# Kernel optimization log

Hardware: AMD Instinct MI355X
Metric: run time of the kernel (lower is better)

The kernel has to match this reference:

```python
import jax, jax.numpy as jnp
import numpy as np

N, B, D = 2048, 4, 512
H, DH = 8, 64
INNER = H * DH
EPS = 1e-5


def _layernorm(x, g, b):
    mu = jnp.mean(x, axis=-1, keepdims=True)
    var = jnp.var(x, axis=-1, keepdims=True)
    return (x - mu) * jax.lax.rsqrt(var + EPS) * g + b


def setup_inputs() -> dict:
    key = jax.random.key(0)
    ks = jax.random.split(key, 5)
    inp = {
        "x": jax.random.normal(ks[0], (N, B, D), jnp.float32),
        "kv": jax.random.normal(ks[1], (N, B, D), jnp.float32),
        # weights stored as [in, out] (jax convention; transpose of torch Linear.weight)
        "Wq": jax.random.normal(ks[2], (D, INNER), jnp.float32) * (D ** -0.5),
        "Wkv": jax.random.normal(ks[3], (D, INNER), jnp.float32) * (D ** -0.5),
        "ln_q_g": jnp.ones((DH,), jnp.float32),
        "ln_q_b": jnp.zeros((DH,), jnp.float32),
        "Wo": jax.random.normal(ks[4], (INNER, D), jnp.float32) * (INNER ** -0.5),
        "bo": jnp.zeros((D,), jnp.float32),
        "ln_o_g": jnp.ones((D,), jnp.float32),
        "ln_o_b": jnp.zeros((D,), jnp.float32),
        "ls_scale": jnp.full((1, 1, D), EPS, jnp.float32),  # LayerScale init eps=1e-5
    }
    return inp


def reference(x, kv, Wq, Wkv, ln_q_g, ln_q_b, Wo, bo, ln_o_g, ln_o_b, ls_scale):
    n = x.shape[0]
    xb = jnp.transpose(x, (1, 0, 2))    # (b, n, d)
    kvb = jnp.transpose(kv, (1, 0, 2))  # (b, m, d)
    b = xb.shape[0]
    q = xb @ Wq                          # (b, n, inner)
    kvp = kvb @ Wkv                      # (b, m, inner)
    q = q.reshape(b, n, H, DH).transpose(0, 2, 1, 3)         # (b, h, n, dh)
    kvp = kvp.reshape(b, -1, H, DH).transpose(0, 2, 1, 3)    # (b, h, m, dh)
    q = _layernorm(q, ln_q_g, ln_q_b)
    sim = jnp.einsum('bhnd,bhmd->bhnm', q, kvp) * (DH ** -0.5)
    attn = jax.nn.softmax(sim, axis=-1)
    out = jnp.einsum('bhnm,bhmd->bhnd', attn, kvp)           # KV shared as value
    out = out.transpose(0, 2, 1, 3).reshape(b, n, INNER)
    out = _layernorm(out @ Wo + bo, ln_o_g, ln_o_b)          # to_out: Linear + LN
    out = jnp.transpose(out, (1, 0, 2))                       # (n, b, d)
    return ls_scale * out
```

## Files before the change

kernel.cpp:

```cpp
#include <hip/hip_runtime.h>

#define NN 2048
#define BB 4
#define DD 512
#define HH 8
#define DHH 64
#define RR 8192

#define SCALE_L2E (0.125f * 1.44269504088896340736f)

typedef __attribute__((ext_vector_type(8))) __bf16 bf16x8;
typedef __attribute__((ext_vector_type(2))) float f32x2;
typedef __attribute__((ext_vector_type(4))) float f32x4;
typedef __attribute__((ext_vector_type(16))) float f32x16;
typedef __attribute__((ext_vector_type(2))) unsigned int u32x2;
typedef __attribute__((ext_vector_type(4))) unsigned int u32x4;

static __device__ __forceinline__ unsigned short f2bf(float f) {
  unsigned u = __builtin_bit_cast(unsigned, f);
  u += 0x7fffu + ((u >> 16) & 1u);
  return (unsigned short)(u >> 16);
}

static __device__ __forceinline__ unsigned cvtpk(float lo, float hi) {
  unsigned r;
  asm("v_cvt_pk_bf16_f32 %0, %1, %2" : "=v"(r) : "v"(lo), "v"(hi));
  return r;
}

#define PAIR(v, i) __builtin_shufflevector(v, v, 2 * (i), 2 * (i) + 1)

static __device__ __forceinline__ void g2l16(const void* g, void* l) {
  __builtin_amdgcn_global_load_lds((const __attribute__((address_space(1))) unsigned int*)g,
                                   (__attribute__((address_space(3))) unsigned int*)l, 16, 0, 0);
}

static __device__ __forceinline__ int swz(int row, int col) {
  return (row * 32 + col) ^ (((row >> 1) & 3) << 3);
}

__global__ __launch_bounds__(256) void cast_all_kernel(
    const float* __restrict__ x, const float* __restrict__ kv,
    const float* __restrict__ Wq, const float* __restrict__ Wkv, const float* __restrict__ Wo,
    unsigned short* __restrict__ xb, unsigned short* __restrict__ kvb,
    unsigned short* __restrict__ WqT, unsigned short* __restrict__ WkvT,
    unsigned short* __restrict__ WoT) {
  int bid = blockIdx.x;
  if (bid < 4096) {
    const float* src = (bid >= 2048) ? kv : x;
    unsigned short* dst = (bid >= 2048) ? kvb : xb;
    int t = (bid & 2047) * 256 + threadIdx.x;
    int o0 = t * 8;
    int d = o0 & 511;
    int n = (o0 >> 9) & 2047;
    int b = o0 >> 20;
    const float* s = src + ((size_t)(n * BB + b) << 9) + d;
    f32x4 v0 = *(const f32x4*)s;
    f32x4 v1 = *(const f32x4*)(s + 4);
    union { unsigned short us[8]; u32x4 v; } o;
#pragma unroll
    for (int i = 0; i < 4; ++i) { o.us[i] = f2bf(v0[i]); o.us[4 + i] = f2bf(v1[i]); }
    *(u32x4*)(dst + o0) = o.v;
  } else {
    int wi = bid - 4096;
    int which = wi >> 10;
    const float* W = (which == 0) ? Wq : (which == 1) ? Wkv : Wo;
    unsigned short* WT = (which == 0) ? WqT : (which == 1) ? WkvT : WoT;
    int idx = (wi & 1023) * 256 + threadIdx.x;
    int o = idx & 511;
    int k = idx >> 9;
    WT[(size_t)o * 512 + k] = f2bf(W[(size_t)k * 512 + o]);
  }
}

#define GEMM_CORE(Aptr, WTptr)                                                        \
  __shared__ unsigned short At[2][128 * 32];                                          \
  __shared__ unsigned short Bt[2][128 * 32];                                          \
  int tid = threadIdx.x;                                                              \
  int w = tid >> 6, l = tid & 63, lr = l & 15, lh = l >> 4;                           \
  int wr = w >> 1, wc = w & 1;                                                        \
  int r0 = blockIdx.x * 128, c0 = blockIdx.y * 128;                                   \
  int chA = w * 2, chB = w * 2 + 1;                                                   \
  int rowA = chA * 16 + (l >> 2), rowB = chB * 16 + (l >> 2);                         \
  int cbA = ((l & 3) * 16) ^ (((rowA >> 1) & 3) << 4);                                \
  int cbB = ((l & 3) * 16) ^ (((rowB >> 1) & 3) << 4);                                \
  const char* sA0 = (const char*)(Aptr) + (size_t)(r0 + rowA) * 1024 + cbA;           \
  const char* sA1 = (const char*)(Aptr) + (size_t)(r0 + rowB) * 1024 + cbB;           \
  const char* sB0 = (const char*)(WTptr) + (size_t)(c0 + rowA) * 1024 + cbA;          \
  const char* sB1 = (const char*)(WTptr) + (size_t)(c0 + rowB) * 1024 + cbB;          \
  auto stageg = [&](int buf, int k0) {                                                \
    char* la = (char*)&At[buf][0] + chA * 1024;                                       \
    char* lb2 = (char*)&Bt[buf][0] + chA * 1024;                                      \
    g2l16(sA0 + k0 * 2, la);                                                          \
    g2l16(sA1 + k0 * 2, la + 1024);                                                   \
    g2l16(sB0 + k0 * 2, lb2);                                                         \
    g2l16(sB1 + k0 * 2, lb2 + 1024);                                                  \
  };                                                                                  \
  f32x4 acc[4][4] = {};                                                               \
  stageg(0, 0);                                                                       \
  __syncthreads();                                                                    \
  _Pragma("unroll")                                                                   \
  for (int i = 0; i < 16; ++i) {                                                      \
    int buf = i & 1;                                                                  \
    if (i < 15) stageg(buf ^ 1, i * 32 + 32);                                         \
    bf16x8 a[4], b[4];                                                                \
    _Pragma("unroll")                                                                 \
    for (int m = 0; m < 4; ++m)                                                       \
      a[m] = *(const bf16x8*)&At[buf][swz(wr * 64 + m * 16 + lr, lh * 8)];            \
    _Pragma("unroll")                                                                 \
    for (int n = 0; n < 4; ++n)                                                       \
      b[n] = *(const bf16x8*)&Bt[buf][swz(wc * 64 + n * 16 + lr, lh * 8)];            \
    _Pragma("unroll")                                                                 \
    for (int m = 0; m < 4; ++m)                                                       \
      _Pragma("unroll")                                                               \
      for (int n = 0; n < 4; ++n)                                                     \
        acc[m][n] = __builtin_amdgcn_mfma_f32_16x16x32_bf16(a[m], b[n], acc[m][n], 0, 0, 0); \
    __syncthreads();                                                                  \
  }

__global__ __launch_bounds__(256) void gemm01_kernel(
    const unsigned short* __restrict__ xb, const unsigned short* __restrict__ kvb,
    const unsigned short* __restrict__ WqT, const unsigned short* __restrict__ WkvT,
    const float* __restrict__ lnqg, const float* __restrict__ lnqb,
    unsigned short* __restrict__ qln, unsigned short* __restrict__ kvp,
    unsigned short* __restrict__ kvpT) {
  int z = blockIdx.z;
  const unsigned short* A = z ? kvb : xb;
  const unsigned short* WT = z ? WkvT : WqT;
  GEMM_CORE(A, WT)
  int row_base = r0 + wr * 64;
  int h = (c0 + wc * 64) >> 6;
  if (z == 0) {
    float gq[4], bq[4];
#pragma unroll
    for (int n = 0; n < 4; ++n) { gq[n] = lnqg[n * 16 + lr]; bq[n] = lnqb[n * 16 + lr]; }
#pragma unroll
    for (int m = 0; m < 4; ++m)
#pragma unroll
      for (int i = 0; i < 4; ++i) {
        float s1 = 0.f, s2 = 0.f;
#pragma unroll
        for (int n = 0; n < 4; ++n) { float v = acc[m][n][i]; s1 += v; s2 += v * v; }
#pragma unroll
        for (int off = 1; off < 16; off <<= 1) { s1 += __shfl_xor(s1, off); s2 += __shfl_xor(s2, off); }
        float mean = s1 * (1.f / 64.f);
        float var = s2 * (1.f / 64.f) - mean * mean;
        float rstd = rsqrtf(var + 1e-5f);
        int row = row_base + m * 16 + lh * 4 + i;
        int b = row >> 11, nidx = row & 2047;
        size_t obase = ((size_t)(b * HH + h) * NN + nidx) * DHH;
#pragma unroll
        for (int n = 0; n < 4; ++n) {
          float v = ((acc[m][n][i] - mean) * rstd * gq[n] + bq[n]) * SCALE_L2E;
          qln[obase + n * 16 + lr] = f2bf(v);
        }
      }
  } else {
#pragma unroll
    for (int m = 0; m < 4; ++m)
#pragma unroll
      for (int i = 0; i < 4; ++i) {
        int row = row_base + m * 16 + lh * 4 + i;
        int b = row >> 11, nidx = row & 2047;
        size_t obase = ((size_t)(b * HH + h) * NN + nidx) * DHH;
        size_t tbase = ((size_t)(b * HH + h) * DHH) * NN + nidx;
#pragma unroll
        for (int n = 0; n < 4; ++n) {
          unsigned short v = f2bf(acc[m][n][i]);
          int dh = n * 16 + lr;
          kvp[obase + dh] = v;
          kvpT[tbase + (size_t)dh * NN] = v;
        }
      }
  }
}

__global__ __launch_bounds__(256) void gemm2_kernel(
    const unsigned short* __restrict__ Ain,
    const unsigned short* __restrict__ WTin,
    const float* __restrict__ g,
    float* __restrict__ out_f32) {
  GEMM_CORE(Ain, WTin)
  int row_base = r0 + wr * 64;
#pragma unroll
  for (int m = 0; m < 4; ++m)
#pragma unroll
    for (int i = 0; i < 4; ++i) {
      int row = row_base + m * 16 + lh * 4 + i;
#pragma unroll
      for (int n = 0; n < 4; ++n) {
        int col = c0 + wc * 64 + n * 16 + lr;
        out_f32[(size_t)row * 512 + col] = acc[m][n][i] + g[col];
      }
    }
}

__global__ __launch_bounds__(128) void attn_kernel(
    const unsigned short* __restrict__ qb, const unsigned short* __restrict__ kb,
    const unsigned short* __restrict__ vtb, unsigned short* __restrict__ attn_out) {
  int bid = blockIdx.x;
  int xcd = bid & 7, idx = bid >> 3;
  int bh = xcd * 4 + (idx >> 5);
  int qt = idx & 31;
  int tid = threadIdx.x, w = tid >> 6, l = tid & 63;
  int q = l & 31, hi = l >> 5;
  const unsigned short* Q = qb + (size_t)bh * NN * DHH;
  const unsigned short* Kp = kb + (size_t)bh * NN * DHH;
  const unsigned short* VT = vtb + (size_t)bh * DHH * NN;
  int qr0 = qt * 64 + w * 32;

  __shared__ unsigned short kt_lds[2][64 * 64];
  __shared__ unsigned short vt_lds[2][64 * 64];

  int qswz = (q & 7) << 4;

  bf16x8 bq[4];
#pragma unroll
  for (int st = 0; st < 4; ++st)
    bq[st] = *(const bf16x8*)&Q[(size_t)(qr0 + q) * DHH + st * 16 + hi * 8];

  float lsum = 0.f;
  f32x16 o0 = {}, o1 = {};

  int rl = l >> 3;
  int scol = ((l & 7) << 4) ^ (rl << 4);
  auto stage = [&](int buf, int kt2) {
    int kr0 = kt2 * 64;
    if (w == 0) {
      char* lb = (char*)&kt_lds[buf][0];
      const char* gb = (const char*)(Kp + (size_t)kr0 * DHH);
#pragma unroll
      for (int p = 0; p < 8; ++p)
        g2l16(gb + (p * 8 + rl) * 128 + scol, lb + p * 1024);
    } else {
      char* lb = (char*)&vt_lds[buf][0];
      const char* gb = (const char*)VT + (size_t)kr0 * 2;
#pragma unroll
      for (int p = 0; p < 8; ++p)
        g2l16(gb + (size_t)(p * 8 + rl) * (NN * 2) + scol, lb + p * 1024);
    }
  };

  stage(0, 0);
  __syncthreads();

#pragma unroll 2
  for (int kt = 0; kt < 32; ++kt) {
    int cur = kt & 1;
    if (kt < 31) stage(cur ^ 1, kt + 1);
    const char* kbuf = (const char*)&kt_lds[cur][0];
    const char* vbuf = (const char*)&vt_lds[cur][0];

    f32x16 s0 = {}, s1 = {};
#pragma unroll
    for (int st = 0; st < 4; ++st) {
      int cb = (st * 32 + hi * 16) ^ qswz;
      bf16x8 a0 = *(const bf16x8*)(kbuf + q * 128 + cb);
      bf16x8 a1 = *(const bf16x8*)(kbuf + (q + 32) * 128 + cb);
      s0 = __builtin_amdgcn_mfma_f32_32x32x16_bf16(a0, bq[st], s0, 0, 0, 0);
      s1 = __builtin_amdgcn_mfma_f32_32x32x16_bf16(a1, bq[st], s1, 0, 0, 0);
    }

#pragma unroll
    for (int i = 0; i < 16; ++i) {
      s0[i] = exp2f(s0[i]);
      s1[i] = exp2f(s1[i]);
    }
    f32x2 t0 = PAIR(s0, 0) + PAIR(s0, 1), t1 = PAIR(s0, 2) + PAIR(s0, 3);
    f32x2 t2 = PAIR(s0, 4) + PAIR(s0, 5), t3 = PAIR(s0, 6) + PAIR(s0, 7);
    f32x2 u0 = PAIR(s1, 0) + PAIR(s1, 1), u1 = PAIR(s1, 2) + PAIR(s1, 3);
    f32x2 u2 = PAIR(s1, 4) + PAIR(s1, 5), u3 = PAIR(s1, 6) + PAIR(s1, 7);
    f32x2 vv = ((t0 + t1) + (t2 + t3)) + ((u0 + u1) + (u2 + u3));
    lsum += vv[0] + vv[1];

#pragma unroll
    for (int st = 0; st < 4; ++st) {
      const f32x16& sv = (st < 2) ? s0 : s1;
      int b0 = (st & 1) * 8;
      unsigned X0 = cvtpk(sv[b0 + 0], sv[b0 + 1]);
      unsigned X1 = cvtpk(sv[b0 + 2], sv[b0 + 3]);
      unsigned Y0 = cvtpk(sv[b0 + 4], sv[b0 + 5]);
      unsigned Y1 = cvtpk(sv[b0 + 6], sv[b0 + 7]);
      auto r0 = __builtin_amdgcn_permlane32_swap(X0, Y0, false, false);
      auto r1 = __builtin_amdgcn_permlane32_swap(X1, Y1, false, false);
      u32x4 pw;
      pw[0] = r0[0];
      pw[1] = r1[0];
      pw[2] = r0[1];
      pw[3] = r1[1];
      bf16x8 bp = __builtin_bit_cast(bf16x8, pw);
      int cb = (st * 32 + hi * 16) ^ qswz;
      bf16x8 va0 = *(const bf16x8*)(vbuf + q * 128 + cb);
      bf16x8 va1 = *(const bf16x8*)(vbuf + (q + 32) * 128 + cb);
      o0 = __builtin_amdgcn_mfma_f32_32x32x16_bf16(va0, bp, o0, 0, 0, 0);
      o1 = __builtin_amdgcn_mfma_f32_32x32x16_bf16(va1, bp, o1, 0, 0, 0);
    }
    __syncthreads();
  }

  lsum += __shfl_xor(lsum, 32);
  float invl = 1.0f / lsum;
  int b = bh >> 3, h = bh & 7;
  size_t base = ((size_t)b * NN + qr0 + q) * 512 + h * 64;
#pragma unroll
  for (int m = 0; m < 4; ++m) {
    u32x2 ov;
    ov[0] = cvtpk(o0[4 * m + 0] * invl, o0[4 * m + 1] * invl);
    ov[1] = cvtpk(o0[4 * m + 2] * invl, o0[4 * m + 3] * invl);
    *(u32x2*)&attn_out[base + m * 8 + hi * 4] = ov;
    ov[0] = cvtpk(o1[4 * m + 0] * invl, o1[4 * m + 1] * invl);
    ov[1] = cvtpk(o1[4 * m + 2] * invl, o1[4 * m + 3] * invl);
    *(u32x2*)&attn_out[base + 32 + m * 8 + hi * 4] = ov;
  }
}

__global__ __launch_bounds__(256) void lnout_kernel(
    const float* __restrict__ proj2, const float* __restrict__ g, const float* __restrict__ beta,
    const float* __restrict__ ls, float* __restrict__ out) {
  int w = threadIdx.x >> 6, l = threadIdx.x & 63;
  int row = blockIdx.x * 4 + w;
  const float* src = proj2 + (size_t)row * DD + l * 8;
  f32x4 v0 = *(const f32x4*)src;
  f32x4 v1 = *(const f32x4*)(src + 4);
  float s1 = 0.f, s2 = 0.f;
#pragma unroll
  for (int i = 0; i < 4; ++i) { s1 += v0[i] + v1[i]; s2 += v0[i] * v0[i] + v1[i] * v1[i]; }
#pragma unroll
  for (int off = 1; off < 64; off <<= 1) { s1 += __shfl_xor(s1, off); s2 += __shfl_xor(s2, off); }
  float mean = s1 * (1.f / 512.f);
  float var = s2 * (1.f / 512.f) - mean * mean;
  float rstd = rsqrtf(var + 1e-5f);
  int b = row >> 11, n = row & 2047;
  float* dst = out + ((size_t)n * BB + b) * DD + l * 8;
  f32x4 r0, r1;
#pragma unroll
  for (int i = 0; i < 4; ++i) {
    int c = l * 8 + i;
    r0[i] = ((v0[i] - mean) * rstd * g[c] + beta[c]) * ls[c];
    int c2 = c + 4;
    r1[i] = ((v1[i] - mean) * rstd * g[c2] + beta[c2]) * ls[c2];
  }
  *(f32x4*)dst = r0;
  *(f32x4*)(dst + 4) = r1;
}

extern "C" void kernel_launch(void* const* d_in, const int* in_sizes, int n_in,
                              void* d_out, int out_size, void* d_ws, size_t ws_size,
                              hipStream_t stream) {
  const float* x = (const float*)d_in[0];
  const float* kv = (const float*)d_in[1];
  const float* Wq = (const float*)d_in[2];
  const float* Wkv = (const float*)d_in[3];
  const float* lnqg = (const float*)d_in[4];
  const float* lnqb = (const float*)d_in[5];
  const float* Wo = (const float*)d_in[6];
  const float* bo = (const float*)d_in[7];
  const float* lnog = (const float*)d_in[8];
  const float* lnob = (const float*)d_in[9];
  const float* ls = (const float*)d_in[10];
  float* out = (float*)d_out;

  unsigned short* xb = (unsigned short*)d_ws;
  unsigned short* kvb = xb + (size_t)RR * DD;
  unsigned short* WqT = kvb + (size_t)RR * DD;
  unsigned short* WkvT = WqT + 512 * 512;
  unsigned short* WoT = WkvT + 512 * 512;
  unsigned short* qln = WoT + 512 * 512;
  unsigned short* kvp = qln + (size_t)RR * DD;
  unsigned short* kvpT = kvp + (size_t)RR * DD;
  unsigned short* aout = kvpT + (size_t)RR * DD;
  float* proj2 = (float*)(aout + (size_t)RR * DD);

  cast_all_kernel<<<dim3(7168), 256, 0, stream>>>(x, kv, Wq, Wkv, Wo, xb, kvb, WqT, WkvT, WoT);
  gemm01_kernel<<<dim3(64, 4, 2), 256, 0, stream>>>(xb, kvb, WqT, WkvT, lnqg, lnqb, qln, kvp, kvpT);
  attn_kernel<<<dim3(1024), 128, 0, stream>>>(qln, kvp, kvpT, aout);
  gemm2_kernel<<<dim3(64, 4), 256, 0, stream>>>(aout, WoT, bo, proj2);
  lnout_kernel<<<dim3(2048), 256, 0, stream>>>(proj2, lnog, lnob, ls, out);
}
```

Measured before the change: 118.0 us.

## Split attention KV range in two across blocks and add reduction kernel

The attention kernel now splits the key/value sequence into two halves, doubling the grid to 2048 blocks. Each block writes unnormalized partial outputs in bf16 plus partial row sums into reused workspace. A new reduce kernel adds the two halves, normalizes, and writes the attention output. This is meant to improve occupancy and load balance on the many-CU GPU, at the cost of an extra launch, partial-result traffic, and bf16 rounding of the partials. The split-sum is correct only because softmax here uses no running max, so the partials can be added directly.

```diff
diff --git a/kernel.cpp b/kernel.cpp
--- a/kernel.cpp
+++ b/kernel.cpp
@@ -197,11 +197,15 @@
 
 __global__ __launch_bounds__(128) void attn_kernel(
     const unsigned short* __restrict__ qb, const unsigned short* __restrict__ kb,
-    const unsigned short* __restrict__ vtb, unsigned short* __restrict__ attn_out) {
+    const unsigned short* __restrict__ vtb,
+    unsigned short* __restrict__ Opart, float* __restrict__ lpart) {
   int bid = blockIdx.x;
   int xcd = bid & 7, idx = bid >> 3;
-  int bh = xcd * 4 + (idx >> 5);
-  int qt = idx & 31;
+  int bh = xcd * 4 + (idx >> 6);
+  int rem = idx & 63;
+  int qt = rem >> 1;
+  int half = rem & 1;
+  int kt0 = half * 16;
   int tid = threadIdx.x, w = tid >> 6, l = tid & 63;
   int q = l & 31, hi = l >> 5;
   const unsigned short* Q = qb + (size_t)bh * NN * DHH;
@@ -241,13 +245,14 @@
     }
   };
 
-  stage(0, 0);
+  stage(0, kt0);
   __syncthreads();
 
 #pragma unroll 2
-  for (int kt = 0; kt < 32; ++kt) {
-    int cur = kt & 1;
-    if (kt < 31) stage(cur ^ 1, kt + 1);
+  for (int it = 0; it < 16; ++it) {
+    int kt = kt0 + it;
+    int cur = it & 1;
+    if (it < 15) stage(cur ^ 1, kt + 1);
     const char* kbuf = (const char*)&kt_lds[cur][0];
     const char* vbuf = (const char*)&vt_lds[cur][0];
 
@@ -299,19 +304,61 @@
   }
 
   lsum += __shfl_xor(lsum, 32);
-  float invl = 1.0f / lsum;
-  int b = bh >> 3, h = bh & 7;
-  size_t base = ((size_t)b * NN + qr0 + q) * 512 + h * 64;
-#pragma unroll
-  for (int m = 0; m < 4; ++m) {
-    u32x2 ov;
-    ov[0] = cvtpk(o0[4 * m + 0] * invl, o0[4 * m + 1] * invl);
-    ov[1] = cvtpk(o0[4 * m + 2] * invl, o0[4 * m + 3] * invl);
-    *(u32x2*)&attn_out[base + m * 8 + hi * 4] = ov;
-    ov[0] = cvtpk(o1[4 * m + 0] * invl, o1[4 * m + 1] * invl);
-    ov[1] = cvtpk(o1[4 * m + 2] * invl, o1[4 * m + 3] * invl);
-    *(u32x2*)&attn_out[base + 32 + m * 8 + hi * 4] = ov;
-  }
+  unsigned short* Ob = Opart + (size_t)bid * 4096;
+  int col = w * 32 + q;
+#pragma unroll
+  for (int r = 0; r < 16; ++r) {
+    int d = (r & 3) + 8 * (r >> 2) + 4 * hi;
+    Ob[d * 64 + col] = f2bf(o0[r]);
+    Ob[(d + 32) * 64 + col] = f2bf(o1[r]);
+  }
+  if (hi == 0) lpart[(size_t)bid * 64 + col] = lsum;
+}
+
+__global__ __launch_bounds__(256) void attn_reduce_kernel(
+    const unsigned short* __restrict__ Opart, const float* __restrict__ lpart,
+    unsigned short* __restrict__ aout) {
+  __shared__ float ldsO[64][65];
+  __shared__ float ldsL[64];
+  int b2 = blockIdx.x;
+  int bh = b2 >> 5, qt = b2 & 31;
+  int j = bh & 3, xcd = bh >> 2;
+  int s0 = (j * 64 + qt * 2) * 8 + xcd;
+  int s1 = s0 + 8;
+  const unsigned short* O0 = Opart + (size_t)s0 * 4096;
+  const unsigned short* O1 = Opart + (size_t)s1 * 4096;
+  int t = threadIdx.x;
+#pragma unroll
+  for (int i = 0; i < 4; ++i) {
+    int e = i * 1024 + t * 4;
+    u32x2 a = *(const u32x2*)(O0 + e);
+    u32x2 b = *(const u32x2*)(O1 + e);
+    int d = e >> 6, qq = e & 63;
+#pragma unroll
+    for (int k2 = 0; k2 < 2; ++k2) {
+      unsigned ua = a[k2], ub = b[k2];
+      float f0 = __builtin_bit_cast(float, (ua & 0xffffu) << 16) +
+                 __builtin_bit_cast(float, (ub & 0xffffu) << 16);
+      float f1 = __builtin_bit_cast(float, ua & 0xffff0000u) +
+                 __builtin_bit_cast(float, ub & 0xffff0000u);
+      ldsO[d][qq + k2 * 2] = f0;
+      ldsO[d][qq + k2 * 2 + 1] = f1;
+    }
+  }
+  if (t < 64) ldsL[t] = lpart[(size_t)s0 * 64 + t] + lpart[(size_t)s1 * 64 + t];
+  __syncthreads();
+  int q = t >> 2, db = (t & 3) * 16;
+  float inv = 1.0f / ldsL[q];
+  unsigned wd[8];
+#pragma unroll
+  for (int p = 0; p < 8; ++p)
+    wd[p] = cvtpk(ldsO[db + 2 * p][q] * inv, ldsO[db + 2 * p + 1][q] * inv);
+  int bbatch = bh >> 3, h = bh & 7;
+  size_t base = ((size_t)bbatch * NN + qt * 64 + q) * 512 + h * 64 + db;
+  u32x4 w0v; w0v[0] = wd[0]; w0v[1] = wd[1]; w0v[2] = wd[2]; w0v[3] = wd[3];
+  u32x4 w1v; w1v[0] = wd[4]; w1v[1] = wd[5]; w1v[2] = wd[6]; w1v[3] = wd[7];
+  *(u32x4*)&aout[base] = w0v;
+  *(u32x4*)&aout[base + 8] = w1v;
 }
 
 __global__ __launch_bounds__(256) void lnout_kernel(
@@ -371,9 +418,13 @@
   unsigned short* aout = kvpT + (size_t)RR * DD;
   float* proj2 = (float*)(aout + (size_t)RR * DD);
 
+  unsigned short* Opart = xb;
+  float* lpart = (float*)WqT;
+
   cast_all_kernel<<<dim3(7168), 256, 0, stream>>>(x, kv, Wq, Wkv, Wo, xb, kvb, WqT, WkvT, WoT);
   gemm01_kernel<<<dim3(64, 4, 2), 256, 0, stream>>>(xb, kvb, WqT, WkvT, lnqg, lnqb, qln, kvp, kvpT);
-  attn_kernel<<<dim3(1024), 128, 0, stream>>>(qln, kvp, kvpT, aout);
+  attn_kernel<<<dim3(2048), 128, 0, stream>>>(qln, kvp, kvpT, Opart, lpart);
+  attn_reduce_kernel<<<dim3(1024), 256, 0, stream>>>(Opart, lpart, aout);
   gemm2_kernel<<<dim3(64, 4), 256, 0, stream>>>(aout, WoT, bo, proj2);
   lnout_kernel<<<dim3(2048), 256, 0, stream>>>(proj2, lnog, lnob, ls, out);
 }
```

Measured after the change: 123.4 us. +4.5%, slower.
